# Performance work log

Measured on AMD Instinct MI355X. Metric: run time of the kernel, lower is better.

Reference implementation:

```python
import jax, jax.numpy as jnp
import numpy as np

B, T, D, L, H = 16, 2048, 512, 6, 1024  # batch, seq, embed_dim, num_layers, mlp hidden (2*D)
K = D // 2  # freq bands; k = min(D//2, T//2) = 256 here
VOCAB = 256


def _ln(x, g, b, eps=1e-5):
    m = x.mean(-1, keepdims=True)
    v = ((x - m) ** 2).mean(-1, keepdims=True)
    return (x - m) / jnp.sqrt(v + eps) * g + b


def setup_inputs() -> dict:
    key = jax.random.key(0)
    ks = jax.random.split(key, 12)
    s = 0.02
    return {
        "byte_ids": jax.random.randint(ks[0], (B, T), 0, 256),
        # ByteSpectralEmbedding params
        "freq_bands": jnp.ones((K,), jnp.float32),
        "fp_w1": jax.random.normal(ks[1], (D, 2 * D), jnp.float32) * s,
        "fp_b1": jnp.zeros((2 * D,), jnp.float32),
        "fp_ln_g": jnp.ones((2 * D,), jnp.float32),
        "fp_ln_b": jnp.zeros((2 * D,), jnp.float32),
        "fp_w2": jax.random.normal(ks[2], (2 * D, D), jnp.float32) * s,
        "fp_b2": jnp.zeros((D,), jnp.float32),
        # SpectralMLPBlock params, stacked over L layers (FNet-style spectral mixing + MLP)
        "blk_ln1_g": jnp.ones((L, D), jnp.float32),
        "blk_ln1_b": jnp.zeros((L, D), jnp.float32),
        "blk_ln2_g": jnp.ones((L, D), jnp.float32),
        "blk_ln2_b": jnp.zeros((L, D), jnp.float32),
        "blk_w1": jax.random.normal(ks[3], (L, D, H), jnp.float32) * s,
        "blk_b1": jnp.zeros((L, H), jnp.float32),
        "blk_w2": jax.random.normal(ks[4], (L, H, D), jnp.float32) * s,
        "blk_b2": jnp.zeros((L, D), jnp.float32),
        # final norm + output head
        "norm_g": jnp.ones((D,), jnp.float32),
        "norm_b": jnp.zeros((D,), jnp.float32),
        "out_w": jax.random.normal(ks[5], (D, VOCAB), jnp.float32) * s,
        "out_b": jnp.zeros((VOCAB,), jnp.float32),
    }


def reference(byte_ids, freq_bands, fp_w1, fp_b1, fp_ln_g, fp_ln_b, fp_w2, fp_b2,
              blk_ln1_g, blk_ln1_b, blk_ln2_g, blk_ln2_b, blk_w1, blk_b1, blk_w2, blk_b2,
              norm_g, norm_b, out_w, out_b):
    Bc, Tc = byte_ids.shape
    k = min(D // 2, Tc // 2)
    signal = byte_ids.astype(jnp.float32) / 127.5 - 1.0          # [B,T]
    X = jnp.fft.fft(signal, axis=1)[:, :k]                        # [B,k] single FFT
    # shift theorem: FFT(roll(signal, -p))[f] = X[f] * exp(+2pi i f p / T)
    mag = jnp.abs(X) * freq_bands[:k]                             # [B,k], position-independent
    base_phase = jnp.angle(X)                                     # [B,k]
    pos = jnp.arange(Tc, dtype=jnp.float32)
    f = jnp.arange(k, dtype=jnp.float32)
    phase = base_phase[:, None, :] + (2.0 * jnp.pi / Tc) * pos[None, :, None] * f[None, None, :]  # [B,T,k]
    mag_bt = jnp.broadcast_to(mag[:, None, :], (Bc, Tc, k))
    feats = jnp.concatenate([mag_bt, jnp.sin(phase), jnp.cos(phase)], axis=-1)
    feats = feats[..., :D] if feats.shape[-1] >= D else jnp.pad(feats, ((0, 0), (0, 0), (0, D - feats.shape[-1])))
    # freq_proj: Linear -> LayerNorm -> GELU -> Linear
    h = feats @ fp_w1 + fp_b1
    h = jax.nn.gelu(_ln(h, fp_ln_g, fp_ln_b), approximate=False)
    x = h @ fp_w2 + fp_b2                                         # [B,T,D]
    # SpectralMLPBlock stack: residual FFT mixing + residual MLP
    for i in range(L):
        y = _ln(x, blk_ln1_g[i], blk_ln1_b[i])
        x = x + jnp.fft.fft(jnp.fft.fft(y, axis=-1), axis=1).real
        y = _ln(x, blk_ln2_g[i], blk_ln2_b[i])
        x = x + jax.nn.gelu(y @ blk_w1[i] + blk_b1[i], approximate=False) @ blk_w2[i] + blk_b2[i]
    x = _ln(x, norm_g, norm_b)
    return x @ out_w + out_b                                      # [B,T,256]
```

## Files before the change

### kernel.cpp

```cpp
#include <hip/hip_runtime.h>
#include <cmath>

typedef unsigned short u16;
typedef unsigned int u32;

constexpr int NB = 16;
constexpr int NT = 2048;
constexpr int ND = 512;
constexpr int NL = 6;
constexpr int NH = 1024;
constexpr int NK = 256;
constexpr int NM = NB * NT;
constexpr int NHALF = NM / 2;

constexpr float PI2 = 6.283185307179586f;

typedef short bf16x8 __attribute__((ext_vector_type(8)));
typedef float f32x4 __attribute__((ext_vector_type(4)));

__device__ __forceinline__ float gelu_exact(float v) {
    return 0.5f * v * (1.0f + erff(v * 0.70710678118654752f));
}

__device__ __forceinline__ u16 f2bf(float f) {
    union { float f; u32 u; } v; v.f = f;
    u32 r = v.u + 0x7FFFu + ((v.u >> 16) & 1u);
    return (u16)(r >> 16);
}

__device__ __forceinline__ float bf2f(u16 h) {
    union { u32 u; float f; } v; v.u = ((u32)h) << 16;
    return v.f;
}

__device__ __forceinline__ float block_sum256(float val, float* lds4) {
#pragma unroll
    for (int o = 32; o > 0; o >>= 1) val += __shfl_down(val, o);
    int lane = threadIdx.x & 63, wid = threadIdx.x >> 6;
    if (lane == 0) lds4[wid] = val;
    __syncthreads();
    float t = lds4[0] + lds4[1] + lds4[2] + lds4[3];
    __syncthreads();
    return t;
}

__global__ void dft_kernel(const int* __restrict__ bytes, const float* __restrict__ fb,
                           float* __restrict__ mag, float* __restrict__ cph,
                           float* __restrict__ sph) {
    __shared__ float lr[4], li[4];
    int b = blockIdx.x, f = blockIdx.y;
    float re = 0.f, im = 0.f;
    for (int t = threadIdx.x; t < NT; t += 256) {
        float s = (float)bytes[b * NT + t] * (1.0f / 127.5f) - 1.0f;
        int idx = (t * f) & (NT - 1);
        float a = (float)idx * (PI2 / NT);
        float sn, cs;
        sincosf(a, &sn, &cs);
        re += s * cs;
        im -= s * sn;
    }
#pragma unroll
    for (int o = 32; o > 0; o >>= 1) {
        re += __shfl_down(re, o);
        im += __shfl_down(im, o);
    }
    int lane = threadIdx.x & 63, wid = threadIdx.x >> 6;
    if (lane == 0) { lr[wid] = re; li[wid] = im; }
    __syncthreads();
    if (threadIdx.x == 0) {
        float R = lr[0] + lr[1] + lr[2] + lr[3];
        float I = li[0] + li[1] + li[2] + li[3];
        float m = sqrtf(R * R + I * I);
        mag[b * NK + f] = m * fb[f];
        float inv = (m > 0.f) ? 1.0f / m : 0.f;
        cph[b * NK + f] = (m > 0.f) ? R * inv : 1.0f;
        sph[b * NK + f] = I * inv;
    }
}

__global__ void feats_split_kernel(const float* __restrict__ mag,
                                   const float* __restrict__ cph,
                                   const float* __restrict__ sph,
                                   u16* __restrict__ hi, u16* __restrict__ lo) {
    int idx = blockIdx.x * 256 + threadIdx.x;
    int d = idx & (ND - 1);
    int m = idx >> 9;
    int b = m >> 11, t = m & (NT - 1);
    float v;
    if (d < NK) {
        v = mag[b * NK + d];
    } else {
        int f = d - NK;
        int a = (t * f) & (NT - 1);
        float sn, cs;
        sincosf((float)a * (PI2 / NT), &sn, &cs);
        v = sph[b * NK + f] * cs + cph[b * NK + f] * sn;
    }
    u16 h = f2bf(v);
    hi[idx] = h;
    lo[idx] = f2bf(v - bf2f(h));
}

template <int NV, int GELU, int OBF>
__global__ void ln_kernel(const float* __restrict__ in, const float* __restrict__ g,
                          const float* __restrict__ bta, void* __restrict__ outv) {
    __shared__ float lds4[4];
    constexpr int NE = NV / 256;
    size_t row = blockIdx.x;
    const float* p = in + row * NV;
    float v[NE];
    float sum = 0.f;
#pragma unroll
    for (int i = 0; i < NE; ++i) {
        v[i] = p[threadIdx.x + 256 * i];
        sum += v[i];
    }
    sum = block_sum256(sum, lds4);
    float mean = sum * (1.0f / NV);
    float sq = 0.f;
#pragma unroll
    for (int i = 0; i < NE; ++i) {
        float d = v[i] - mean;
        sq += d * d;
    }
    sq = block_sum256(sq, lds4);
    float inv = rsqrtf(sq * (1.0f / NV) + 1e-5f);
#pragma unroll
    for (int i = 0; i < NE; ++i) {
        int c = threadIdx.x + 256 * i;
        float r = (v[i] - mean) * inv * g[c] + bta[c];
        if (GELU) r = gelu_exact(r);
        if (OBF == 2) {
            u16* o = (u16*)outv + row * (2 * NV);
            u16 hb = f2bf(r);
            o[c] = hb;
            o[NV + c] = f2bf(r - bf2f(hb));
        } else if (OBF == 1) {
            ((u16*)outv)[row * NV + c] = f2bf(r);
        } else {
            ((float*)outv)[row * NV + c] = r;
        }
    }
}

__global__ void ln_fftd_kernel(const float* __restrict__ x, const float* __restrict__ g,
                               const float* __restrict__ bta, float* __restrict__ P,
                               int row_base) {
    __shared__ float sr[2][512], si[2][512];
    __shared__ float red[2][2];
    int sub = threadIdx.x >> 7;
    int tid = threadIdx.x & 127;
    int rlocal = blockIdx.x * 2 + sub;
    const float* p = x + ((size_t)row_base + rlocal) * ND;
    float v[4];
    float s = 0.f;
#pragma unroll
    for (int j = 0; j < 4; ++j) { v[j] = p[tid + 128 * j]; s += v[j]; }
#pragma unroll
    for (int o = 32; o > 0; o >>= 1) s += __shfl_down(s, o);
    int wv = (threadIdx.x >> 6) & 1;
    if ((threadIdx.x & 63) == 0) red[sub][wv] = s;
    __syncthreads();
    float mean = (red[sub][0] + red[sub][1]) * (1.0f / ND);
    float q = 0.f;
#pragma unroll
    for (int j = 0; j < 4; ++j) { float d = v[j] - mean; q += d * d; }
#pragma unroll
    for (int o = 32; o > 0; o >>= 1) q += __shfl_down(q, o);
    __syncthreads();
    if ((threadIdx.x & 63) == 0) red[sub][wv] = q;
    __syncthreads();
    float inv = rsqrtf((red[sub][0] + red[sub][1]) * (1.0f / ND) + 1e-5f);
#pragma unroll
    for (int j = 0; j < 4; ++j) {
        int i = tid + 128 * j;
        int r = __brev((unsigned)i) >> 23;
        sr[sub][r] = (v[j] - mean) * inv * g[i] + bta[i];
        si[sub][r] = 0.f;
    }
    __syncthreads();
    for (int len = 2; len <= 512; len <<= 1) {
        int half = len >> 1;
        for (int qq = tid; qq < 256; qq += 128) {
            int k = qq & (half - 1);
            int j = ((qq - k) << 1) + k;
            float a = -PI2 * (float)k / (float)len;
            float sn = __sinf(a), cs = __cosf(a);
            float ur = sr[sub][j], ui = si[sub][j];
            float vr = sr[sub][j + half], vi = si[sub][j + half];
            float tr = vr * cs - vi * sn;
            float ti = vr * sn + vi * cs;
            sr[sub][j] = ur + tr;
            si[sub][j] = ui + ti;
            sr[sub][j + half] = ur - tr;
            si[sub][j + half] = ui - ti;
        }
        __syncthreads();
    }
    float* out = P + (size_t)rlocal * ND;
    for (int i = tid; i < 512; i += 128)
        out[i] = (i <= 256) ? sr[sub][i] : si[sub][i - 256];
}

__global__ void transpose_bt_kernel(const float* __restrict__ P, float* __restrict__ PT) {
    __shared__ float tile[32][33];
    int b = blockIdx.z, t0 = blockIdx.x * 32, d0 = blockIdx.y * 32;
    int j = threadIdx.x & 31, i0 = threadIdx.x >> 5;
    for (int i = i0; i < 32; i += 8)
        tile[i][j] = P[((size_t)(b * NT + t0 + i)) * ND + d0 + j];
    __syncthreads();
    for (int i = i0; i < 32; i += 8)
        PT[((size_t)(b * ND + d0 + i)) * NT + t0 + j] = tile[j][i];
}

__global__ void fft_t2048_kernel(const float* __restrict__ PT, float* __restrict__ Mt) {
    __shared__ float sr[2048], si[2048];
    int b = blockIdx.x;
    int d = blockIdx.y;
    const float* zr = PT + ((size_t)(b * ND + d)) * NT;
    const float* zi = PT + ((size_t)(b * ND + 256 + d)) * NT;
    bool has_im = (d != 0) && (d != 256);
    for (int t = threadIdx.x; t < 2048; t += 256) {
        int r = __brev((unsigned)t) >> 21;
        sr[r] = zr[t];
        si[r] = has_im ? zi[t] : 0.f;
    }
    __syncthreads();
    for (int len = 2; len <= 2048; len <<= 1) {
        int half = len >> 1;
        for (int q = threadIdx.x; q < 1024; q += 256) {
            int k = q & (half - 1);
            int j = ((q - k) << 1) + k;
            float a = -PI2 * (float)k / (float)len;
            float sn = __sinf(a), cs = __cosf(a);
            float ur = sr[j], ui = si[j];
            float vr = sr[j + half], vi = si[j + half];
            float tr = vr * cs - vi * sn;
            float ti = vr * sn + vi * cs;
            sr[j] = ur + tr;
            si[j] = ui + ti;
            sr[j + half] = ur - tr;
            si[j + half] = ui - ti;
        }
        __syncthreads();
    }
    float* m0 = Mt + ((size_t)(b * ND + d)) * NT;
    for (int t = threadIdx.x; t < 2048; t += 256) m0[t] = sr[t];
    if (has_im) {
        float* m1 = Mt + ((size_t)(b * ND + (512 - d))) * NT;
        for (int t = threadIdx.x; t < 2048; t += 256) m1[t] = sr[(2048 - t) & 2047];
    }
}

__global__ void add_transpose_kernel(const float* __restrict__ Mt, float* __restrict__ x) {
    __shared__ float tile[32][33];
    int b = blockIdx.z, t0 = blockIdx.x * 32, d0 = blockIdx.y * 32;
    int j = threadIdx.x & 31, i0 = threadIdx.x >> 5;
    for (int i = i0; i < 32; i += 8)
        tile[i][j] = Mt[((size_t)(b * ND + d0 + i)) * NT + t0 + j];
    __syncthreads();
    for (int i = i0; i < 32; i += 8) {
        size_t xi = ((size_t)(b * NT + t0 + i)) * ND + d0 + j;
        x[xi] += tile[j][i];
    }
}

__global__ void wconv_kernel(const float* __restrict__ W, u16* __restrict__ Wt,
                             int K, int N) {
    __shared__ float tile[32][33];
    size_t moff = (size_t)blockIdx.z * K * N;
    int n0 = blockIdx.x * 32, k0 = blockIdx.y * 32;
    int j = threadIdx.x & 31, i0 = threadIdx.x >> 5;
    for (int i = i0; i < 32; i += 8)
        tile[i][j] = W[moff + (size_t)(k0 + i) * N + n0 + j];
    __syncthreads();
    for (int i = i0; i < 32; i += 8)
        Wt[moff + (size_t)(n0 + i) * K + k0 + j] = f2bf(tile[j][i]);
}

template <int GELU, int ACC, int OBF, int ADDB>
__global__ __launch_bounds__(256) void mfma_gemm(
    const u16* __restrict__ A, int lda, const u16* __restrict__ Wt,
    const float* __restrict__ bias, void* __restrict__ Cv, int Kd, int Nd) {
    __shared__ __align__(16) u16 Al[2][4096];
    __shared__ __align__(16) u16 Bl[2][4096];
    int tid = threadIdx.x;
    int row0 = blockIdx.x * 128, col0 = blockIdx.y * 128;
    int lane = tid & 63, w = tid >> 6;
    int wr = w >> 1, wc = w & 1;
    int kg = lane >> 4, ln16 = lane & 15;

    f32x4 acc[4][4] = {};

    auto stage = [&](int buf, int k0) {
#pragma unroll
        for (int i = 0; i < 2; ++i) {
            int s = i * 256 + tid;
            int skg = s >> 7, r = s & 127;
            const u16* ga = A + (size_t)(row0 + r) * lda + k0 + skg * 8;
            __builtin_amdgcn_global_load_lds(
                (const __attribute__((address_space(1))) void*)ga,
                (__attribute__((address_space(3))) void*)&Al[buf][s * 8], 16, 0, 0);
            const u16* gb = Wt + (size_t)(col0 + r) * Kd + k0 + skg * 8;
            __builtin_amdgcn_global_load_lds(
                (const __attribute__((address_space(1))) void*)gb,
                (__attribute__((address_space(3))) void*)&Bl[buf][s * 8], 16, 0, 0);
        }
    };
    auto compute = [&](int buf) {
        bf16x8 af[4], bfr[4];
#pragma unroll
        for (int mi = 0; mi < 4; ++mi)
            af[mi] = *(const bf16x8*)&Al[buf][(kg * 128 + wr * 64 + mi * 16 + ln16) * 8];
#pragma unroll
        for (int ni = 0; ni < 4; ++ni)
            bfr[ni] = *(const bf16x8*)&Bl[buf][(kg * 128 + wc * 64 + ni * 16 + ln16) * 8];
#pragma unroll
        for (int mi = 0; mi < 4; ++mi)
#pragma unroll
            for (int ni = 0; ni < 4; ++ni)
                acc[mi][ni] = __builtin_amdgcn_mfma_f32_16x16x32_bf16(
                    af[mi], bfr[ni], acc[mi][ni], 0, 0, 0);
    };

    int nt = Kd >> 5;
    stage(0, 0);
    __syncthreads();
    int cur = 0;
    for (int t = 1; t < nt; ++t) {
        stage(cur ^ 1, t << 5);
        compute(cur);
        __syncthreads();
        cur ^= 1;
    }
    compute(cur);

#pragma unroll
    for (int mi = 0; mi < 4; ++mi) {
#pragma unroll
        for (int ni = 0; ni < 4; ++ni) {
            int col = col0 + wc * 64 + ni * 16 + ln16;
            float bv = ADDB ? bias[col] : 0.f;
#pragma unroll
            for (int j = 0; j < 4; ++j) {
                int row = row0 + wr * 64 + mi * 16 + kg * 4 + j;
                float v = acc[mi][ni][j] + bv;
                if (GELU) v = gelu_exact(v);
                size_t o = (size_t)row * Nd + col;
                if (OBF) {
                    ((u16*)Cv)[o] = f2bf(v);
                } else {
                    float* C = (float*)Cv;
                    if (ACC) v += C[o];
                    C[o] = v;
                }
            }
        }
    }
}

__global__ __launch_bounds__(256) void mfma_gemm2(
    const u16* __restrict__ Ahi, const u16* __restrict__ Alo, int lda,
    const u16* __restrict__ Wt, const float* __restrict__ bias,
    float* __restrict__ C, int Kd, int Nd) {
    __shared__ __align__(16) u16 Ah[2][4096];
    __shared__ __align__(16) u16 Al2[2][4096];
    __shared__ __align__(16) u16 Bl[2][4096];
    int tid = threadIdx.x;
    int row0 = blockIdx.x * 128, col0 = blockIdx.y * 128;
    int lane = tid & 63, w = tid >> 6;
    int wr = w >> 1, wc = w & 1;
    int kg = lane >> 4, ln16 = lane & 15;

    f32x4 acc[4][4] = {};

    auto stage = [&](int buf, int k0) {
#pragma unroll
        for (int i = 0; i < 2; ++i) {
            int s = i * 256 + tid;
            int skg = s >> 7, r = s & 127;
            size_t aoff = (size_t)(row0 + r) * lda + k0 + skg * 8;
            __builtin_amdgcn_global_load_lds(
                (const __attribute__((address_space(1))) void*)(Ahi + aoff),
                (__attribute__((address_space(3))) void*)&Ah[buf][s * 8], 16, 0, 0);
            __builtin_amdgcn_global_load_lds(
                (const __attribute__((address_space(1))) void*)(Alo + aoff),
                (__attribute__((address_space(3))) void*)&Al2[buf][s * 8], 16, 0, 0);
            const u16* gb = Wt + (size_t)(col0 + r) * Kd + k0 + skg * 8;
            __builtin_amdgcn_global_load_lds(
                (const __attribute__((address_space(1))) void*)gb,
                (__attribute__((address_space(3))) void*)&Bl[buf][s * 8], 16, 0, 0);
        }
    };
    auto compute = [&](int buf) {
        bf16x8 ah[4], al[4], bfr[4];
#pragma unroll
        for (int mi = 0; mi < 4; ++mi) {
            int sl = (kg * 128 + wr * 64 + mi * 16 + ln16) * 8;
            ah[mi] = *(const bf16x8*)&Ah[buf][sl];
            al[mi] = *(const bf16x8*)&Al2[buf][sl];
        }
#pragma unroll
        for (int ni = 0; ni < 4; ++ni)
            bfr[ni] = *(const bf16x8*)&Bl[buf][(kg * 128 + wc * 64 + ni * 16 + ln16) * 8];
#pragma unroll
        for (int mi = 0; mi < 4; ++mi)
#pragma unroll
            for (int ni = 0; ni < 4; ++ni) {
                acc[mi][ni] = __builtin_amdgcn_mfma_f32_16x16x32_bf16(
                    ah[mi], bfr[ni], acc[mi][ni], 0, 0, 0);
                acc[mi][ni] = __builtin_amdgcn_mfma_f32_16x16x32_bf16(
                    al[mi], bfr[ni], acc[mi][ni], 0, 0, 0);
            }
    };

    int nt = Kd >> 5;
    stage(0, 0);
    __syncthreads();
    int cur = 0;
    for (int t = 1; t < nt; ++t) {
        stage(cur ^ 1, t << 5);
        compute(cur);
        __syncthreads();
        cur ^= 1;
    }
    compute(cur);

#pragma unroll
    for (int mi = 0; mi < 4; ++mi) {
#pragma unroll
        for (int ni = 0; ni < 4; ++ni) {
            int col = col0 + wc * 64 + ni * 16 + ln16;
            float bv = bias[col];
#pragma unroll
            for (int j = 0; j < 4; ++j) {
                int row = row0 + wr * 64 + mi * 16 + kg * 4 + j;
                C[(size_t)row * Nd + col] = acc[mi][ni][j] + bv;
            }
        }
    }
}

extern "C" void kernel_launch(void* const* d_in, const int* in_sizes, int n_in,
                              void* d_out, int out_size, void* d_ws, size_t ws_size,
                              hipStream_t stream) {
    const int* byte_ids     = (const int*)d_in[0];
    const float* freq_bands = (const float*)d_in[1];
    const float* fp_w1   = (const float*)d_in[2];
    const float* fp_b1   = (const float*)d_in[3];
    const float* fp_ln_g = (const float*)d_in[4];
    const float* fp_ln_b = (const float*)d_in[5];
    const float* fp_w2   = (const float*)d_in[6];
    const float* fp_b2   = (const float*)d_in[7];
    const float* blk_ln1_g = (const float*)d_in[8];
    const float* blk_ln1_b = (const float*)d_in[9];
    const float* blk_ln2_g = (const float*)d_in[10];
    const float* blk_ln2_b = (const float*)d_in[11];
    const float* blk_w1  = (const float*)d_in[12];
    const float* blk_b1  = (const float*)d_in[13];
    const float* blk_w2  = (const float*)d_in[14];
    const float* blk_b2  = (const float*)d_in[15];
    const float* norm_g  = (const float*)d_in[16];
    const float* norm_b  = (const float*)d_in[17];
    const float* out_w   = (const float*)d_in[18];
    const float* out_b   = (const float*)d_in[19];
    float* out = (float*)d_out;
    char* base = (char*)d_ws;
    const size_t MB = 1048576;

    u16* fhi     = (u16*)base;
    u16* flo     = (u16*)(base + 32 * MB);
    float* xA    = (float*)base;
    float* hfp   = (float*)(base + 64 * MB);
    u16* h2      = (u16*)hfp;
    float* Zbuf  = (float*)(base + 64 * MB);
    float* PTbuf = (float*)(base + 96 * MB);
    float* Mtbuf = Zbuf;
    u16* hmlp    = (u16*)(base + 64 * MB);
    u16* ybf     = (u16*)(base + 128 * MB);
    u16* wbase   = (u16*)(base + 160 * MB);
    u16* blkw1t  = wbase;
    u16* blkw2t  = wbase + 3145728;
    u16* outwt   = wbase + 6291456;
    u16* fpw1t   = (u16*)d_out;
    u16* fpw2t   = (u16*)((char*)d_out + 1 * MB);
    float* mag   = (float*)((char*)d_out + 2 * MB);
    float* cph   = mag + NB * NK;
    float* sph   = cph + NB * NK;

    dft_kernel<<<dim3(NB, NK), 256, 0, stream>>>(byte_ids, freq_bands, mag, cph, sph);
    feats_split_kernel<<<(NM * ND) / 256, 256, 0, stream>>>(mag, cph, sph, fhi, flo);
    wconv_kernel<<<dim3(NH / 32, ND / 32, 1), 256, 0, stream>>>(fp_w1, fpw1t, ND, NH);
    wconv_kernel<<<dim3(ND / 32, NH / 32, 1), 256, 0, stream>>>(fp_w2, fpw2t, NH, ND);

    mfma_gemm2<<<dim3(NM / 128, NH / 128), 256, 0, stream>>>(
        fhi, flo, ND, fpw1t, fp_b1, hfp, ND, NH);
    ln_kernel<NH, 1, 2><<<NM, 256, 0, stream>>>(hfp, fp_ln_g, fp_ln_b, h2);
    mfma_gemm2<<<dim3(NM / 128, ND / 128), 256, 0, stream>>>(
        h2, h2 + NH, 2 * NH, fpw2t, fp_b2, xA, NH, ND);

    wconv_kernel<<<dim3(NH / 32, ND / 32, NL), 256, 0, stream>>>(blk_w1, blkw1t, ND, NH);
    wconv_kernel<<<dim3(ND / 32, NH / 32, NL), 256, 0, stream>>>(blk_w2, blkw2t, NH, ND);
    wconv_kernel<<<dim3(256 / 32, ND / 32, 1), 256, 0, stream>>>(out_w, outwt, ND, 256);

    for (int l = 0; l < NL; ++l) {
        for (int hh = 0; hh < 2; ++hh) {
            int row_base = hh * NHALF;
            ln_fftd_kernel<<<NHALF / 2, 256, 0, stream>>>(
                xA, blk_ln1_g + l * ND, blk_ln1_b + l * ND, Zbuf, row_base);
            transpose_bt_kernel<<<dim3(NT / 32, ND / 32, 8), 256, 0, stream>>>(Zbuf, PTbuf);
            fft_t2048_kernel<<<dim3(8, 257), 256, 0, stream>>>(PTbuf, Mtbuf);
            add_transpose_kernel<<<dim3(NT / 32, ND / 32, 8), 256, 0, stream>>>(
                Mtbuf, xA + (size_t)row_base * ND);
        }
        ln_kernel<ND, 0, 1><<<NM, 256, 0, stream>>>(
            xA, blk_ln2_g + l * ND, blk_ln2_b + l * ND, ybf);
        mfma_gemm<1, 0, 1, 1><<<dim3(NM / 128, NH / 128), 256, 0, stream>>>(
            ybf, ND, blkw1t + (size_t)l * ND * NH, blk_b1 + l * NH, hmlp, ND, NH);
        mfma_gemm<0, 1, 0, 1><<<dim3(NM / 128, ND / 128), 256, 0, stream>>>(
            hmlp, NH, blkw2t + (size_t)l * ND * NH, blk_b2 + l * ND, xA, NH, ND);
    }

    ln_kernel<ND, 0, 1><<<NM, 256, 0, stream>>>(xA, norm_g, norm_b, ybf);
    mfma_gemm<0, 0, 0, 1><<<dim3(NM / 128, 256 / 128), 256, 0, stream>>>(
        ybf, ND, outwt, out_b, out, ND, 256);
}
```

Baseline: 3.221 ms.

## Triple-buffer GEMM K-loop with vmcnt waits and swizzle workgroups across XCDs

Both MFMA GEMM kernels move from a double-buffered loop to a three-stage ring of LDS buffers. Loads for tile t+2 are issued before computing tile t, and partial s_waitcnt vmcnt counts let later loads stay in flight while a single barrier guards each step. A block-index remap groups workgroups across the eight XCDs so blocks sharing A/W tiles likely share L2. This raises LDS use per block, which may reduce occupancy, and it relies on hand-counted vmcnt values being correct.

Measured after the change: 3.226 ms. About the same (+0.1%).

```diff
diff --git a/kernel.cpp b/kernel.cpp
--- a/kernel.cpp
+++ b/kernel.cpp
@@ -42,6 +42,19 @@
     float t = lds4[0] + lds4[1] + lds4[2] + lds4[3];
     __syncthreads();
     return t;
+}
+
+__device__ __forceinline__ void swz_block(int& row0, int& col0) {
+    int nwg = gridDim.x * gridDim.y;
+    int wg = blockIdx.x + blockIdx.y * gridDim.x;
+    int L = wg;
+    if ((nwg & 7) == 0) {
+        int q = nwg >> 3;
+        L = (wg & 7) * q + (wg >> 3);
+    }
+    int ncol = gridDim.y;
+    row0 = (L / ncol) * 128;
+    col0 = (L % ncol) * 128;
 }
 
 __global__ void dft_kernel(const int* __restrict__ bytes, const float* __restrict__ fb,
@@ -282,17 +295,19 @@
 __global__ __launch_bounds__(256) void mfma_gemm(
     const u16* __restrict__ A, int lda, const u16* __restrict__ Wt,
     const float* __restrict__ bias, void* __restrict__ Cv, int Kd, int Nd) {
-    __shared__ __align__(16) u16 Al[2][4096];
-    __shared__ __align__(16) u16 Bl[2][4096];
+    __shared__ __align__(16) u16 Al[3][4096];
+    __shared__ __align__(16) u16 Bl[3][4096];
     int tid = threadIdx.x;
-    int row0 = blockIdx.x * 128, col0 = blockIdx.y * 128;
+    int row0, col0;
+    swz_block(row0, col0);
     int lane = tid & 63, w = tid >> 6;
     int wr = w >> 1, wc = w & 1;
     int kg = lane >> 4, ln16 = lane & 15;
 
     f32x4 acc[4][4] = {};
 
-    auto stage = [&](int buf, int k0) {
+    auto stage = [&](int buf, int t) {
+        int k0 = t << 5;
 #pragma unroll
         for (int i = 0; i < 2; ++i) {
             int s = i * 256 + tid;
@@ -325,15 +340,16 @@
 
     int nt = Kd >> 5;
     stage(0, 0);
-    __syncthreads();
-    int cur = 0;
-    for (int t = 1; t < nt; ++t) {
-        stage(cur ^ 1, t << 5);
-        compute(cur);
-        __syncthreads();
-        cur ^= 1;
-    }
-    compute(cur);
+    stage(1, 1);
+    for (int t = 0; t < nt; ++t) {
+        if (t + 1 < nt) asm volatile("s_waitcnt vmcnt(4)" ::: "memory");
+        else            asm volatile("s_waitcnt vmcnt(0)" ::: "memory");
+        __builtin_amdgcn_sched_barrier(0);
+        __builtin_amdgcn_s_barrier();
+        __builtin_amdgcn_sched_barrier(0);
+        if (t + 2 < nt) stage((t + 2) % 3, t + 2);
+        compute(t % 3);
+    }
 
 #pragma unroll
     for (int mi = 0; mi < 4; ++mi) {
@@ -363,18 +379,20 @@
     const u16* __restrict__ Ahi, const u16* __restrict__ Alo, int lda,
     const u16* __restrict__ Wt, const float* __restrict__ bias,
     float* __restrict__ C, int Kd, int Nd) {
-    __shared__ __align__(16) u16 Ah[2][4096];
-    __shared__ __align__(16) u16 Al2[2][4096];
-    __shared__ __align__(16) u16 Bl[2][4096];
+    __shared__ __align__(16) u16 Ah[3][4096];
+    __shared__ __align__(16) u16 Al2[3][4096];
+    __shared__ __align__(16) u16 Bl[3][4096];
     int tid = threadIdx.x;
-    int row0 = blockIdx.x * 128, col0 = blockIdx.y * 128;
+    int row0, col0;
+    swz_block(row0, col0);
     int lane = tid & 63, w = tid >> 6;
     int wr = w >> 1, wc = w & 1;
     int kg = lane >> 4, ln16 = lane & 15;
 
     f32x4 acc[4][4] = {};
 
-    auto stage = [&](int buf, int k0) {
+    auto stage = [&](int buf, int t) {
+        int k0 = t << 5;
 #pragma unroll
         for (int i = 0; i < 2; ++i) {
             int s = i * 256 + tid;
@@ -416,15 +434,16 @@
 
     int nt = Kd >> 5;
     stage(0, 0);
-    __syncthreads();
-    int cur = 0;
-    for (int t = 1; t < nt; ++t) {
-        stage(cur ^ 1, t << 5);
-        compute(cur);
-        __syncthreads();
-        cur ^= 1;
-    }
-    compute(cur);
+    stage(1, 1);
+    for (int t = 0; t < nt; ++t) {
+        if (t + 1 < nt) asm volatile("s_waitcnt vmcnt(6)" ::: "memory");
+        else            asm volatile("s_waitcnt vmcnt(0)" ::: "memory");
+        __builtin_amdgcn_sched_barrier(0);
+        __builtin_amdgcn_s_barrier();
+        __builtin_amdgcn_sched_barrier(0);
+        if (t + 2 < nt) stage((t + 2) % 3, t + 2);
+        compute(t % 3);
+    }
 
 #pragma unroll
     for (int mi = 0; mi < 4; ++mi) {
```
